# Performance work log

Hardware: AMD Instinct MI355X
Metric: run time of the kernel (lower is better)

The kernel has to match this reference:

```python
import jax, jax.numpy as jnp
import numpy as np

N_NODES = 50000
N_EDGES = 800000
F_IN = 256
HID = 128
HEADS = 4
F_OUT = 64
NEG_SLOPE = 0.2


def setup_inputs() -> dict:
    key = jax.random.key(0)
    ks = jax.random.split(key, 12)
    x = jax.random.normal(ks[0], (N_NODES, F_IN), dtype=jnp.float32)
    edge_index = jax.random.randint(ks[1], (2, N_EDGES), 0, N_NODES, dtype=jnp.int64)
    s = 0.05
    return {
        "x": x,
        "edge_index": edge_index,
        "W1": jax.random.normal(ks[2], (F_IN, HEADS * HID), dtype=jnp.float32) * s,
        "a_src1": jax.random.normal(ks[3], (HEADS, HID), dtype=jnp.float32) * s,
        "a_dst1": jax.random.normal(ks[4], (HEADS, HID), dtype=jnp.float32) * s,
        "b1": jnp.zeros((HEADS * HID,), dtype=jnp.float32),
        "W2": jax.random.normal(ks[5], (HEADS * HID, F_OUT), dtype=jnp.float32) * s,
        "a_src2": jax.random.normal(ks[6], (1, F_OUT), dtype=jnp.float32) * s,
        "a_dst2": jax.random.normal(ks[7], (1, F_OUT), dtype=jnp.float32) * s,
        "b2": jnp.zeros((F_OUT,), dtype=jnp.float32),
    }


def _add_self_loops(edge_index, n):
    loop = jnp.arange(n, dtype=edge_index.dtype)
    return jnp.concatenate([edge_index, jnp.stack([loop, loop])], axis=1)


def _gat_conv(x, edge_index, W, a_src, a_dst, bias, heads, out_ch):
    # PyG GATConv: h = x @ W reshaped to [N, H, C]
    n = x.shape[0]
    h = (x @ W).reshape(n, heads, out_ch)
    # per-node attention logits [N, H]
    al_src = jnp.einsum('nhc,hc->nh', h, a_src)
    al_dst = jnp.einsum('nhc,hc->nh', h, a_dst)
    src, dst = edge_index[0], edge_index[1]
    e = jax.nn.leaky_relu(al_src[src] + al_dst[dst], NEG_SLOPE)  # [E, H]
    # softmax over incoming edges per destination node (segment softmax)
    e_max = jax.ops.segment_max(e, dst, num_segments=n)
    e_exp = jnp.exp(e - e_max[dst])
    denom = jax.ops.segment_sum(e_exp, dst, num_segments=n)
    alpha = e_exp / (denom[dst] + 1e-16)  # [E, H]
    msg = h[src] * alpha[:, :, None]  # [E, H, C]
    out = jax.ops.segment_sum(msg, dst, num_segments=n)  # [N, H, C]
    return out.reshape(n, heads * out_ch) + bias


def reference(x, edge_index, W1, a_src1, a_dst1, b1, W2, a_src2, a_dst2, b2):
    # Dropout layers are identity in eval mode.
    ei = _add_self_loops(edge_index, x.shape[0])
    h = jax.nn.elu(_gat_conv(x, ei, W1, a_src1, a_dst1, b1, HEADS, HID))
    out = _gat_conv(h, ei, W2, a_src2, a_dst2, b2, 1, F_OUT)
    return out
```

## Files before the change

kernel.cpp:

```cpp
#include <hip/hip_runtime.h>
#include <math.h>

#define N_NODES 50000
#define N_EDGES 800000
#define E_TOT   850000
#define F_IN    256
#define F1      512
#define HID     128
#define HEADS   4
#define F_OUT   64

typedef __attribute__((ext_vector_type(8))) short short8;
typedef __attribute__((ext_vector_type(4))) float f32x4;
typedef unsigned short ushort_t;
typedef unsigned int uint_t;

__device__ __forceinline__ float lrelu(float x){ return x > 0.f ? x : 0.2f*x; }
__device__ __forceinline__ float elu(float x){ return x > 0.f ? x : expm1f(x); }

__device__ __forceinline__ ushort_t f2b(float f){
  uint_t u = __builtin_bit_cast(uint_t, f);
  u += 0x7fffu + ((u >> 16) & 1u);
  return (ushort_t)(u >> 16);
}
__device__ __forceinline__ float blo(uint_t u){ return __builtin_bit_cast(float, u << 16); }
__device__ __forceinline__ float bhi(uint_t u){ return __builtin_bit_cast(float, u & 0xffff0000u); }
__device__ __forceinline__ float b2f(ushort_t s){ return __builtin_bit_cast(float, (uint_t)s << 16); }

__global__ void hist_kernel(const int* __restrict__ ei, int* __restrict__ deg16){
  int e = blockIdx.x*blockDim.x + threadIdx.x;
  if (e >= E_TOT) return;
  int dst = (e < N_EDGES) ? ei[N_EDGES + e] : (e - N_EDGES);
  atomicAdd(&deg16[dst*16], 1);
}

__global__ __launch_bounds__(256) void scan1_kernel(const int* __restrict__ deg16,
                                                    int* __restrict__ offs,
                                                    int* __restrict__ bsum){
  __shared__ int sd[256];
  const int tid = threadIdx.x;
  const int i = blockIdx.x*256 + tid;
  int v = (i < N_NODES) ? deg16[i*16] : 0;
  sd[tid] = v; __syncthreads();
  #pragma unroll
  for (int off = 1; off < 256; off <<= 1){
    int t = (tid >= off) ? sd[tid - off] : 0;
    __syncthreads();
    sd[tid] += t;
    __syncthreads();
  }
  if (i < N_NODES) offs[i] = sd[tid] - v;
  if (tid == 255) bsum[blockIdx.x] = sd[255];
}

__global__ __launch_bounds__(256) void scan2_kernel(const int* __restrict__ bsum,
                                                    int* __restrict__ bbase, int nb){
  __shared__ int sd[256];
  const int tid = threadIdx.x;
  int v = (tid < nb) ? bsum[tid] : 0;
  sd[tid] = v; __syncthreads();
  #pragma unroll
  for (int off = 1; off < 256; off <<= 1){
    int t = (tid >= off) ? sd[tid - off] : 0;
    __syncthreads();
    sd[tid] += t;
    __syncthreads();
  }
  if (tid < nb) bbase[tid] = sd[tid] - v;
}

__global__ __launch_bounds__(256) void scan3_kernel(int* __restrict__ offs,
                                                    const int* __restrict__ bbase,
                                                    int* __restrict__ cur16){
  const int i = blockIdx.x*256 + threadIdx.x;
  if (i < N_NODES){
    int o = offs[i] + bbase[blockIdx.x];
    offs[i] = o;
    cur16[i*16] = o;
  }
  if (blockIdx.x == 0 && threadIdx.x == 0) offs[N_NODES] = E_TOT;
}

__global__ void scatter_kernel(const int* __restrict__ ei, int* __restrict__ cur16,
                               int* __restrict__ ssrc){
  int e = blockIdx.x*blockDim.x + threadIdx.x;
  if (e >= E_TOT) return;
  int src, dst;
  if (e < N_EDGES){ src = ei[e]; dst = ei[N_EDGES + e]; }
  else            { src = e - N_EDGES; dst = src; }
  int pos = atomicAdd(&cur16[dst*16], 1);
  ssrc[pos] = src;
}

__global__ __launch_bounds__(256) void cvt_x_kernel(const float* __restrict__ x,
                                                    ushort_t* __restrict__ xb){
  const int t = blockIdx.x*256 + threadIdx.x;
  const float4 a = ((const float4*)x)[t*2];
  const float4 b = ((const float4*)x)[t*2 + 1];
  uint4 o;
  o.x = (uint_t)f2b(a.x) | ((uint_t)f2b(a.y) << 16);
  o.y = (uint_t)f2b(a.z) | ((uint_t)f2b(a.w) << 16);
  o.z = (uint_t)f2b(b.x) | ((uint_t)f2b(b.y) << 16);
  o.w = (uint_t)f2b(b.z) | ((uint_t)f2b(b.w) << 16);
  ((uint4*)xb)[t] = o;
}

__global__ __launch_bounds__(256) void transpose_bf16_kernel(const float* __restrict__ W,
                                                             ushort_t* __restrict__ Wt,
                                                             int K, int N){
  __shared__ float tile[64][65];
  const int k0 = blockIdx.x*64, n0 = blockIdx.y*64;
  const int c = threadIdx.x & 63, r4 = threadIdx.x >> 6;
  for (int r = r4; r < 64; r += 4)
    tile[r][c] = W[(size_t)(k0 + r)*N + n0 + c];
  __syncthreads();
  for (int r = r4; r < 64; r += 4)
    Wt[(size_t)(n0 + r)*K + k0 + c] = f2b(tile[c][r]);
}

template<int K, int WR, int WC>
__global__ __launch_bounds__(256) void gemm_bf16(const ushort_t* __restrict__ A,
                                                 const ushort_t* __restrict__ Bt,
                                                 ushort_t* __restrict__ C,
                                                 int M, int N){
  constexpr int BM = WR*64, BN = WC*64, BKP = 40;
  __shared__ ushort_t As[BM*BKP];
  __shared__ ushort_t Bs[BN*BKP];
  const int tid = threadIdx.x;
  const int wave = tid >> 6, lane = tid & 63, quad = lane >> 4, l16 = lane & 15;
  const int wm = wave % WR, wn = wave / WR;
  const int m0 = blockIdx.x*BM, n0 = blockIdx.y*BN;
  f32x4 acc[4][4] = {};
  for (int k0 = 0; k0 < K; k0 += 32){
    #pragma unroll
    for (int s = tid; s < BM*4; s += 256){
      int r = s >> 2, c = s & 3;
      int gr = m0 + r; if (gr >= M) gr = M - 1;
      *(uint4*)(As + r*BKP + c*8) = *(const uint4*)(A + (size_t)gr*K + k0 + c*8);
    }
    #pragma unroll
    for (int s = tid; s < BN*4; s += 256){
      int r = s >> 2, c = s & 3;
      *(uint4*)(Bs + r*BKP + c*8) = *(const uint4*)(Bt + (size_t)(n0 + r)*K + k0 + c*8);
    }
    __syncthreads();
    short8 af[4], bfr[4];
    #pragma unroll
    for (int i = 0; i < 4; ++i)
      af[i] = *(const short8*)(As + (wm*64 + i*16 + l16)*BKP + quad*8);
    #pragma unroll
    for (int j = 0; j < 4; ++j)
      bfr[j] = *(const short8*)(Bs + (wn*64 + j*16 + l16)*BKP + quad*8);
    #pragma unroll
    for (int i = 0; i < 4; ++i)
      #pragma unroll
      for (int j = 0; j < 4; ++j)
        acc[i][j] = __builtin_amdgcn_mfma_f32_16x16x32_bf16(af[i], bfr[j], acc[i][j], 0, 0, 0);
    __syncthreads();
  }
  #pragma unroll
  for (int i = 0; i < 4; ++i){
    #pragma unroll
    for (int r = 0; r < 4; ++r){
      int row = m0 + wm*64 + i*16 + quad*4 + r;
      if (row < M){
        #pragma unroll
        for (int j = 0; j < 4; ++j){
          int col = n0 + wn*64 + j*16 + l16;
          C[(size_t)row*N + col] = f2b(acc[i][j][r]);
        }
      }
    }
  }
}

__global__ __launch_bounds__(128) void logits1_kernel(const ushort_t* __restrict__ h1b,
                                                      const float* __restrict__ a_src,
                                                      const float* __restrict__ a_dst,
                                                      float* __restrict__ als,
                                                      float* __restrict__ ald){
  const int n = blockIdx.x;
  const int tid = threadIdx.x;
  const int head = tid >> 5, p = tid & 31;
  const uint2 v = *(const uint2*)(h1b + (size_t)n*F1 + tid*4);
  float h0 = blo(v.x), h1 = bhi(v.x), h2 = blo(v.y), h3 = bhi(v.y);
  const float4 as = *(const float4*)(a_src + head*HID + p*4);
  const float4 ad = *(const float4*)(a_dst + head*HID + p*4);
  float ds = h0*as.x + h1*as.y + h2*as.z + h3*as.w;
  float dd = h0*ad.x + h1*ad.y + h2*ad.z + h3*ad.w;
  #pragma unroll
  for (int off = 16; off >= 1; off >>= 1){
    ds += __shfl_down(ds, off, 32);
    dd += __shfl_down(dd, off, 32);
  }
  if (p == 0){ als[n*4 + head] = ds; ald[n*4 + head] = dd; }
}

#define FMA8(hv, al) do{ \
  acc[0] = fmaf(blo((hv).x), (al), acc[0]); \
  acc[1] = fmaf(bhi((hv).x), (al), acc[1]); \
  acc[2] = fmaf(blo((hv).y), (al), acc[2]); \
  acc[3] = fmaf(bhi((hv).y), (al), acc[3]); \
  acc[4] = fmaf(blo((hv).z), (al), acc[4]); \
  acc[5] = fmaf(bhi((hv).z), (al), acc[5]); \
  acc[6] = fmaf(blo((hv).w), (al), acc[6]); \
  acc[7] = fmaf(bhi((hv).w), (al), acc[7]); }while(0)

__global__ __launch_bounds__(256) void agg1_kernel(const ushort_t* __restrict__ h1b,
                                                   const float* __restrict__ als,
                                                   const float* __restrict__ ald1,
                                                   const float* __restrict__ b1,
                                                   const int* __restrict__ offs,
                                                   const int* __restrict__ ssrc,
                                                   ushort_t* __restrict__ hb){
  __shared__ int   shsrc[4][64];
  __shared__ float shal[4][64][4];
  const int wave = threadIdx.x >> 6, lane = threadIdx.x & 63;
  const int n = blockIdx.x*4 + wave;
  const int head = lane >> 4;
  const float4 ald = ((const float4*)ald1)[n];
  const int s0 = offs[n], s1 = offs[n+1];
  const int nE = s1 - s0;

  float acc[8] = {0.f,0.f,0.f,0.f,0.f,0.f,0.f,0.f};

  if (nE <= 64){
    float4 a4 = {0.f,0.f,0.f,0.f};
    int sc = 0;
    if (lane < nE){
      sc = ssrc[s0 + lane];
      const float4 as = ((const float4*)als)[sc];
      a4.x = __expf(lrelu(as.x + ald.x));
      a4.y = __expf(lrelu(as.y + ald.y));
      a4.z = __expf(lrelu(as.z + ald.z));
      a4.w = __expf(lrelu(as.w + ald.w));
    }
    shsrc[wave][lane] = sc;
    *(float4*)&shal[wave][lane][0] = a4;

    const ushort_t* hbase = h1b + lane*8;
    const int nE4 = (nE + 3) & ~3;
    float dsum = 0.f;

    uint4 h0  = *(const uint4*)(hbase + ((size_t)shsrc[wave][0] << 9));
    uint4 h1v = *(const uint4*)(hbase + ((size_t)shsrc[wave][1] << 9));
    uint4 h2v = *(const uint4*)(hbase + ((size_t)shsrc[wave][2] << 9));
    uint4 h3v = *(const uint4*)(hbase + ((size_t)shsrc[wave][3] << 9));
    float al0 = shal[wave][0][head];
    float al1 = shal[wave][1][head];
    float al2 = shal[wave][2][head];
    float al3 = shal[wave][3][head];
    for (int k = 0; k < nE4; k += 4){
      uint4 p0 = h0, p1 = h1v, p2 = h2v, p3 = h3v;
      float q0 = 0.f, q1 = 0.f, q2 = 0.f, q3 = 0.f;
      if (k + 4 < nE4){
        p0 = *(const uint4*)(hbase + ((size_t)shsrc[wave][k+4] << 9));
        p1 = *(const uint4*)(hbase + ((size_t)shsrc[wave][k+5] << 9));
        p2 = *(const uint4*)(hbase + ((size_t)shsrc[wave][k+6] << 9));
        p3 = *(const uint4*)(hbase + ((size_t)shsrc[wave][k+7] << 9));
        q0 = shal[wave][k+4][head];
        q1 = shal[wave][k+5][head];
        q2 = shal[wave][k+6][head];
        q3 = shal[wave][k+7][head];
      }
      dsum += (al0 + al1) + (al2 + al3);
      FMA8(h0,  al0);
      FMA8(h1v, al1);
      FMA8(h2v, al2);
      FMA8(h3v, al3);
      h0 = p0; h1v = p1; h2v = p2; h3v = p3;
      al0 = q0; al1 = q1; al2 = q2; al3 = q3;
    }

    const float rd = 1.0f / (dsum + 1e-16f);
    const float4 ba = *(const float4*)(b1 + lane*8);
    const float4 bb = *(const float4*)(b1 + lane*8 + 4);
    float o0 = elu(fmaf(acc[0], rd, ba.x)), o1 = elu(fmaf(acc[1], rd, ba.y));
    float o2 = elu(fmaf(acc[2], rd, ba.z)), o3 = elu(fmaf(acc[3], rd, ba.w));
    float o4 = elu(fmaf(acc[4], rd, bb.x)), o5 = elu(fmaf(acc[5], rd, bb.y));
    float o6 = elu(fmaf(acc[6], rd, bb.z)), o7 = elu(fmaf(acc[7], rd, bb.w));
    uint4 o;
    o.x = (uint_t)f2b(o0) | ((uint_t)f2b(o1) << 16);
    o.y = (uint_t)f2b(o2) | ((uint_t)f2b(o3) << 16);
    o.z = (uint_t)f2b(o4) | ((uint_t)f2b(o5) << 16);
    o.w = (uint_t)f2b(o6) | ((uint_t)f2b(o7) << 16);
    *(uint4*)(hb + (size_t)n*F1 + lane*8) = o;
    return;
  }

  float d0 = 0.f, d1 = 0.f, d2 = 0.f, d3 = 0.f;
  for (int e = s0 + lane; e < s1; e += 64){
    const int sc = ssrc[e];
    const float4 as = ((const float4*)als)[sc];
    d0 += __expf(lrelu(as.x + ald.x));
    d1 += __expf(lrelu(as.y + ald.y));
    d2 += __expf(lrelu(as.z + ald.z));
    d3 += __expf(lrelu(as.w + ald.w));
  }
  #pragma unroll
  for (int off = 32; off >= 1; off >>= 1){
    d0 += __shfl_xor(d0, off);
    d1 += __shfl_xor(d1, off);
    d2 += __shfl_xor(d2, off);
    d3 += __shfl_xor(d3, off);
  }
  const float den = (head == 0) ? d0 : (head == 1) ? d1 : (head == 2) ? d2 : d3;
  const float rd = 1.0f / (den + 1e-16f);

  for (int ce = s0; ce < s1; ce += 64){
    const int idx = ce + lane;
    if (idx < s1){
      const int sc = ssrc[idx];
      const float4 as = ((const float4*)als)[sc];
      shsrc[wave][lane] = sc;
      float4 a4;
      a4.x = __expf(lrelu(as.x + ald.x));
      a4.y = __expf(lrelu(as.y + ald.y));
      a4.z = __expf(lrelu(as.z + ald.z));
      a4.w = __expf(lrelu(as.w + ald.w));
      *(float4*)&shal[wave][lane][0] = a4;
    }
    const int nB = min(64, s1 - ce);
    for (int k = 0; k < nB; ++k){
      const int scb = shsrc[wave][k];
      const float al = shal[wave][k][head] * rd;
      const uint4 hv = *(const uint4*)(h1b + (size_t)scb*F1 + lane*8);
      FMA8(hv, al);
    }
  }
  const float4 ba = *(const float4*)(b1 + lane*8);
  const float4 bb = *(const float4*)(b1 + lane*8 + 4);
  float o0 = elu(acc[0] + ba.x), o1 = elu(acc[1] + ba.y);
  float o2 = elu(acc[2] + ba.z), o3 = elu(acc[3] + ba.w);
  float o4 = elu(acc[4] + bb.x), o5 = elu(acc[5] + bb.y);
  float o6 = elu(acc[6] + bb.z), o7 = elu(acc[7] + bb.w);
  uint4 o;
  o.x = (uint_t)f2b(o0) | ((uint_t)f2b(o1) << 16);
  o.y = (uint_t)f2b(o2) | ((uint_t)f2b(o3) << 16);
  o.z = (uint_t)f2b(o4) | ((uint_t)f2b(o5) << 16);
  o.w = (uint_t)f2b(o6) | ((uint_t)f2b(o7) << 16);
  *(uint4*)(hb + (size_t)n*F1 + lane*8) = o;
}

__global__ __launch_bounds__(64) void logits2_kernel(const ushort_t* __restrict__ gb,
                                                     const float* __restrict__ a_src,
                                                     const float* __restrict__ a_dst,
                                                     float* __restrict__ als,
                                                     float* __restrict__ ald){
  const int n = blockIdx.x;
  const int tid = threadIdx.x;
  const float v = b2f(gb[(size_t)n*F_OUT + tid]);
  float ds = v * a_src[tid];
  float dd = v * a_dst[tid];
  #pragma unroll
  for (int off = 32; off >= 1; off >>= 1){
    ds += __shfl_xor(ds, off);
    dd += __shfl_xor(dd, off);
  }
  if (tid == 0){ als[n] = ds; ald[n] = dd; }
}

__global__ __launch_bounds__(256) void agg2_kernel(const ushort_t* __restrict__ gb,
                                                   const float* __restrict__ als,
                                                   const float* __restrict__ ald2,
                                                   const float* __restrict__ b2,
                                                   const int* __restrict__ offs,
                                                   const int* __restrict__ ssrc,
                                                   float* __restrict__ out){
  __shared__ int   shsrc[4][64];
  __shared__ float shal[4][64];
  const int wave = threadIdx.x >> 6, lane = threadIdx.x & 63;
  const int n = blockIdx.x*4 + wave;
  const float ald = ald2[n];
  const int s0 = offs[n], s1 = offs[n+1];
  const int nE = s1 - s0;

  if (nE <= 64){
    float av = 0.f; int sc = 0;
    if (lane < nE){
      sc = ssrc[s0 + lane];
      av = __expf(lrelu(als[sc] + ald));
    }
    shsrc[wave][lane] = sc;
    shal[wave][lane] = av;

    const int half = lane >> 5;
    const int ch2  = lane & 31;
    float acc0 = 0.f, acc1 = 0.f, dsum = 0.f;
    for (int k = half; k < nE; k += 2){
      const int scb  = shsrc[wave][k];
      const float al = shal[wave][k];
      const uint_t v = *(const uint_t*)(gb + ((size_t)scb << 6) + ch2*2);
      acc0 = fmaf(blo(v), al, acc0);
      acc1 = fmaf(bhi(v), al, acc1);
      dsum += al;
    }
    acc0 += __shfl_xor(acc0, 32);
    acc1 += __shfl_xor(acc1, 32);
    dsum += __shfl_xor(dsum, 32);
    const float rd = 1.0f / (dsum + 1e-16f);
    if (lane < 32){
      const float2 bb = *(const float2*)(b2 + ch2*2);
      float2 o2;
      o2.x = fmaf(acc0, rd, bb.x);
      o2.y = fmaf(acc1, rd, bb.y);
      *(float2*)(out + (size_t)n*F_OUT + ch2*2) = o2;
    }
    return;
  }

  float dsum = 0.f;
  for (int e = s0 + lane; e < s1; e += 64)
    dsum += __expf(lrelu(als[ssrc[e]] + ald));
  #pragma unroll
  for (int off = 32; off >= 1; off >>= 1)
    dsum += __shfl_xor(dsum, off);
  const float rd = 1.0f / (dsum + 1e-16f);

  float acc = 0.f;
  for (int ce = s0; ce < s1; ce += 64){
    const int idx = ce + lane;
    if (idx < s1){
      const int sc = ssrc[idx];
      shsrc[wave][lane] = sc;
      shal[wave][lane] = __expf(lrelu(als[sc] + ald)) * rd;
    }
    const int nB = min(64, s1 - ce);
    for (int k = 0; k < nB; ++k){
      const int scb = shsrc[wave][k];
      const float al = shal[wave][k];
      acc = fmaf(b2f(gb[(size_t)scb*F_OUT + lane]), al, acc);
    }
  }
  out[(size_t)n*F_OUT + lane] = acc + b2[lane];
}

#undef FMA8

extern "C" void kernel_launch(void* const* d_in, const int* in_sizes, int n_in,
                              void* d_out, int out_size, void* d_ws, size_t ws_size,
                              hipStream_t stream){
  const float* x      = (const float*)d_in[0];
  const int*   ei     = (const int*)  d_in[1];
  const float* W1     = (const float*)d_in[2];
  const float* a_src1 = (const float*)d_in[3];
  const float* a_dst1 = (const float*)d_in[4];
  const float* b1     = (const float*)d_in[5];
  const float* W2     = (const float*)d_in[6];
  const float* a_src2 = (const float*)d_in[7];
  const float* a_dst2 = (const float*)d_in[8];
  const float* b2     = (const float*)d_in[9];
  float* out = (float*)d_out;

  char* ws = (char*)d_ws;
  ushort_t* h1b  = (ushort_t*)(ws + 0UL);
  ushort_t* hb   = (ushort_t*)(ws + 51200000UL);
  ushort_t* xb   = (ushort_t*)(ws + 102400000UL);
  ushort_t* gb   = (ushort_t*)(ws + 128000000UL);
  ushort_t* W1t  = (ushort_t*)(ws + 134400000UL);
  ushort_t* W2t  = (ushort_t*)(ws + 134662144UL);
  float*    als1 = (float*)   (ws + 134727680UL);
  float*    ald1 = (float*)   (ws + 135527680UL);
  float*    als2 = (float*)   (ws + 136327680UL);
  float*    ald2 = (float*)   (ws + 136527680UL);
  int*      offs = (int*)     (ws + 136927680UL);
  int*      bsum = (int*)     (ws + 137127744UL);
  int*      bbase= (int*)     (ws + 137128544UL);
  int*      ssrc = (int*)     (ws + 137329600UL);

  int*      deg16 = (int*)    (ws + 51200000UL);
  int*      cur16 = (int*)    (ws + 54400000UL);

  hipMemsetAsync(deg16, 0, 3200000, stream);

  const int eb = (E_TOT + 255) / 256;
  const int nb = (N_NODES + 255) / 256;
  hist_kernel   <<<eb, 256, 0, stream>>>(ei, deg16);
  scan1_kernel  <<<nb, 256, 0, stream>>>(deg16, offs, bsum);
  scan2_kernel  <<<1, 256, 0, stream>>>(bsum, bbase, nb);
  scan3_kernel  <<<nb, 256, 0, stream>>>(offs, bbase, cur16);
  scatter_kernel<<<eb, 256, 0, stream>>>(ei, cur16, ssrc);

  cvt_x_kernel        <<<6250, 256, 0, stream>>>(x, xb);
  transpose_bf16_kernel<<<dim3(4, 8), 256, 0, stream>>>(W1, W1t, F_IN, F1);
  transpose_bf16_kernel<<<dim3(8, 1), 256, 0, stream>>>(W2, W2t, F1, F_OUT);

  gemm_bf16<F_IN, 2, 2><<<dim3(391, 4), 256, 0, stream>>>(xb, W1t, h1b, N_NODES, F1);
  logits1_kernel<<<N_NODES, 128, 0, stream>>>(h1b, a_src1, a_dst1, als1, ald1);
  agg1_kernel   <<<12500, 256, 0, stream>>>(h1b, als1, ald1, b1, offs, ssrc, hb);

  gemm_bf16<F1, 4, 1><<<dim3(196, 1), 256, 0, stream>>>(hb, W2t, gb, N_NODES, F_OUT);
  logits2_kernel<<<N_NODES, 64, 0, stream>>>(gb, a_src2, a_dst2, als2, ald2);
  agg2_kernel   <<<12500, 256, 0, stream>>>(gb, als2, ald2, b2, offs, ssrc, out);
}
```

Measured before the change: 475.2 us.

## Split layer-1 aggregation into alpha precompute and channel-sliced gather kernel

Replaces the fused layer-1 attention-aggregation kernel with two kernels. The first computes normalized softmax weights per edge and head into a workspace buffer that reuses the x-bf16 region. The second gathers neighbour features in 64-channel slices, with each block covering 16 nodes for one slice, so each gathered row segment is smaller and there are more independent blocks. The cost is an extra pass that writes and then rereads the alpha array. Each lane also now loads 4 bytes per gathered row instead of 16, which adds load instructions.

```diff
diff --git a/kernel.cpp b/kernel.cpp
--- a/kernel.cpp
+++ b/kernel.cpp
@@ -196,95 +196,43 @@
   if (p == 0){ als[n*4 + head] = ds; ald[n*4 + head] = dd; }
 }
 
-#define FMA8(hv, al) do{ \
-  acc[0] = fmaf(blo((hv).x), (al), acc[0]); \
-  acc[1] = fmaf(bhi((hv).x), (al), acc[1]); \
-  acc[2] = fmaf(blo((hv).y), (al), acc[2]); \
-  acc[3] = fmaf(bhi((hv).y), (al), acc[3]); \
-  acc[4] = fmaf(blo((hv).z), (al), acc[4]); \
-  acc[5] = fmaf(bhi((hv).z), (al), acc[5]); \
-  acc[6] = fmaf(blo((hv).w), (al), acc[6]); \
-  acc[7] = fmaf(bhi((hv).w), (al), acc[7]); }while(0)
-
-__global__ __launch_bounds__(256) void agg1_kernel(const ushort_t* __restrict__ h1b,
-                                                   const float* __restrict__ als,
-                                                   const float* __restrict__ ald1,
-                                                   const float* __restrict__ b1,
-                                                   const int* __restrict__ offs,
-                                                   const int* __restrict__ ssrc,
-                                                   ushort_t* __restrict__ hb){
-  __shared__ int   shsrc[4][64];
-  __shared__ float shal[4][64][4];
+__global__ __launch_bounds__(256) void alpha1_kernel(const float* __restrict__ als,
+                                                     const float* __restrict__ ald1,
+                                                     const int* __restrict__ offs,
+                                                     const int* __restrict__ ssrc,
+                                                     float* __restrict__ alpha){
   const int wave = threadIdx.x >> 6, lane = threadIdx.x & 63;
   const int n = blockIdx.x*4 + wave;
-  const int head = lane >> 4;
   const float4 ald = ((const float4*)ald1)[n];
   const int s0 = offs[n], s1 = offs[n+1];
   const int nE = s1 - s0;
 
-  float acc[8] = {0.f,0.f,0.f,0.f,0.f,0.f,0.f,0.f};
-
   if (nE <= 64){
-    float4 a4 = {0.f,0.f,0.f,0.f};
-    int sc = 0;
-    if (lane < nE){
-      sc = ssrc[s0 + lane];
+    float e0 = 0.f, e1 = 0.f, e2 = 0.f, e3 = 0.f;
+    const int idx = s0 + lane;
+    const bool act = lane < nE;
+    if (act){
+      const int sc = ssrc[idx];
       const float4 as = ((const float4*)als)[sc];
-      a4.x = __expf(lrelu(as.x + ald.x));
-      a4.y = __expf(lrelu(as.y + ald.y));
-      a4.z = __expf(lrelu(as.z + ald.z));
-      a4.w = __expf(lrelu(as.w + ald.w));
-    }
-    shsrc[wave][lane] = sc;
-    *(float4*)&shal[wave][lane][0] = a4;
-
-    const ushort_t* hbase = h1b + lane*8;
-    const int nE4 = (nE + 3) & ~3;
-    float dsum = 0.f;
-
-    uint4 h0  = *(const uint4*)(hbase + ((size_t)shsrc[wave][0] << 9));
-    uint4 h1v = *(const uint4*)(hbase + ((size_t)shsrc[wave][1] << 9));
-    uint4 h2v = *(const uint4*)(hbase + ((size_t)shsrc[wave][2] << 9));
-    uint4 h3v = *(const uint4*)(hbase + ((size_t)shsrc[wave][3] << 9));
-    float al0 = shal[wave][0][head];
-    float al1 = shal[wave][1][head];
-    float al2 = shal[wave][2][head];
-    float al3 = shal[wave][3][head];
-    for (int k = 0; k < nE4; k += 4){
-      uint4 p0 = h0, p1 = h1v, p2 = h2v, p3 = h3v;
-      float q0 = 0.f, q1 = 0.f, q2 = 0.f, q3 = 0.f;
-      if (k + 4 < nE4){
-        p0 = *(const uint4*)(hbase + ((size_t)shsrc[wave][k+4] << 9));
-        p1 = *(const uint4*)(hbase + ((size_t)shsrc[wave][k+5] << 9));
-        p2 = *(const uint4*)(hbase + ((size_t)shsrc[wave][k+6] << 9));
-        p3 = *(const uint4*)(hbase + ((size_t)shsrc[wave][k+7] << 9));
-        q0 = shal[wave][k+4][head];
-        q1 = shal[wave][k+5][head];
-        q2 = shal[wave][k+6][head];
-        q3 = shal[wave][k+7][head];
-      }
-      dsum += (al0 + al1) + (al2 + al3);
-      FMA8(h0,  al0);
-      FMA8(h1v, al1);
-      FMA8(h2v, al2);
-      FMA8(h3v, al3);
-      h0 = p0; h1v = p1; h2v = p2; h3v = p3;
-      al0 = q0; al1 = q1; al2 = q2; al3 = q3;
-    }
-
-    const float rd = 1.0f / (dsum + 1e-16f);
-    const float4 ba = *(const float4*)(b1 + lane*8);
-    const float4 bb = *(const float4*)(b1 + lane*8 + 4);
-    float o0 = elu(fmaf(acc[0], rd, ba.x)), o1 = elu(fmaf(acc[1], rd, ba.y));
-    float o2 = elu(fmaf(acc[2], rd, ba.z)), o3 = elu(fmaf(acc[3], rd, ba.w));
-    float o4 = elu(fmaf(acc[4], rd, bb.x)), o5 = elu(fmaf(acc[5], rd, bb.y));
-    float o6 = elu(fmaf(acc[6], rd, bb.z)), o7 = elu(fmaf(acc[7], rd, bb.w));
-    uint4 o;
-    o.x = (uint_t)f2b(o0) | ((uint_t)f2b(o1) << 16);
-    o.y = (uint_t)f2b(o2) | ((uint_t)f2b(o3) << 16);
-    o.z = (uint_t)f2b(o4) | ((uint_t)f2b(o5) << 16);
-    o.w = (uint_t)f2b(o6) | ((uint_t)f2b(o7) << 16);
-    *(uint4*)(hb + (size_t)n*F1 + lane*8) = o;
+      e0 = __expf(lrelu(as.x + ald.x));
+      e1 = __expf(lrelu(as.y + ald.y));
+      e2 = __expf(lrelu(as.z + ald.z));
+      e3 = __expf(lrelu(as.w + ald.w));
+    }
+    float d0 = e0, d1 = e1, d2 = e2, d3 = e3;
+    #pragma unroll
+    for (int off = 32; off >= 1; off >>= 1){
+      d0 += __shfl_xor(d0, off);
+      d1 += __shfl_xor(d1, off);
+      d2 += __shfl_xor(d2, off);
+      d3 += __shfl_xor(d3, off);
+    }
+    if (act){
+      alpha[0*E_TOT + idx] = e0 / (d0 + 1e-16f);
+      alpha[1*E_TOT + idx] = e1 / (d1 + 1e-16f);
+      alpha[2*E_TOT + idx] = e2 / (d2 + 1e-16f);
+      alpha[3*E_TOT + idx] = e3 / (d3 + 1e-16f);
+    }
     return;
   }
 
@@ -304,42 +252,82 @@
     d2 += __shfl_xor(d2, off);
     d3 += __shfl_xor(d3, off);
   }
-  const float den = (head == 0) ? d0 : (head == 1) ? d1 : (head == 2) ? d2 : d3;
-  const float rd = 1.0f / (den + 1e-16f);
-
-  for (int ce = s0; ce < s1; ce += 64){
-    const int idx = ce + lane;
-    if (idx < s1){
-      const int sc = ssrc[idx];
-      const float4 as = ((const float4*)als)[sc];
-      shsrc[wave][lane] = sc;
-      float4 a4;
-      a4.x = __expf(lrelu(as.x + ald.x));
-      a4.y = __expf(lrelu(as.y + ald.y));
-      a4.z = __expf(lrelu(as.z + ald.z));
-      a4.w = __expf(lrelu(as.w + ald.w));
-      *(float4*)&shal[wave][lane][0] = a4;
-    }
-    const int nB = min(64, s1 - ce);
-    for (int k = 0; k < nB; ++k){
-      const int scb = shsrc[wave][k];
-      const float al = shal[wave][k][head] * rd;
-      const uint4 hv = *(const uint4*)(h1b + (size_t)scb*F1 + lane*8);
-      FMA8(hv, al);
-    }
-  }
-  const float4 ba = *(const float4*)(b1 + lane*8);
-  const float4 bb = *(const float4*)(b1 + lane*8 + 4);
-  float o0 = elu(acc[0] + ba.x), o1 = elu(acc[1] + ba.y);
-  float o2 = elu(acc[2] + ba.z), o3 = elu(acc[3] + ba.w);
-  float o4 = elu(acc[4] + bb.x), o5 = elu(acc[5] + bb.y);
-  float o6 = elu(acc[6] + bb.z), o7 = elu(acc[7] + bb.w);
-  uint4 o;
-  o.x = (uint_t)f2b(o0) | ((uint_t)f2b(o1) << 16);
-  o.y = (uint_t)f2b(o2) | ((uint_t)f2b(o3) << 16);
-  o.z = (uint_t)f2b(o4) | ((uint_t)f2b(o5) << 16);
-  o.w = (uint_t)f2b(o6) | ((uint_t)f2b(o7) << 16);
-  *(uint4*)(hb + (size_t)n*F1 + lane*8) = o;
+  const float r0 = 1.f/(d0+1e-16f), r1 = 1.f/(d1+1e-16f);
+  const float r2 = 1.f/(d2+1e-16f), r3 = 1.f/(d3+1e-16f);
+  for (int e = s0 + lane; e < s1; e += 64){
+    const int sc = ssrc[e];
+    const float4 as = ((const float4*)als)[sc];
+    alpha[0*E_TOT + e] = __expf(lrelu(as.x + ald.x)) * r0;
+    alpha[1*E_TOT + e] = __expf(lrelu(as.y + ald.y)) * r1;
+    alpha[2*E_TOT + e] = __expf(lrelu(as.z + ald.z)) * r2;
+    alpha[3*E_TOT + e] = __expf(lrelu(as.w + ald.w)) * r3;
+  }
+}
+
+__global__ __launch_bounds__(256) void agg1s_kernel(const ushort_t* __restrict__ h1b,
+                                                    const float* __restrict__ alpha,
+                                                    const float* __restrict__ b1,
+                                                    const int* __restrict__ offs,
+                                                    const int* __restrict__ ssrc,
+                                                    ushort_t* __restrict__ hb){
+  __shared__ int   shsrc[4][64];
+  __shared__ float shal[4][64];
+  const int wave = threadIdx.x >> 6, lane = threadIdx.x & 63;
+  const int s = blockIdx.x & 7;
+  const int g = blockIdx.x >> 3;
+  const int head = s >> 1;
+  const float* aplane = alpha + (size_t)head*E_TOT;
+  const int half = lane >> 5, ch2 = lane & 31;
+  const ushort_t* hcol = h1b + s*64 + ch2*2;
+  float2 bb = {0.f, 0.f};
+  if (lane < 32) bb = *(const float2*)(b1 + s*64 + ch2*2);
+
+  #pragma unroll
+  for (int q = 0; q < 4; ++q){
+    const int n = g*16 + wave*4 + q;
+    const int s0 = offs[n], s1v = offs[n+1];
+    const int nE = s1v - s0;
+    float acc0 = 0.f, acc1 = 0.f;
+
+    if (nE <= 64){
+      if (lane < nE){
+        shsrc[wave][lane] = ssrc[s0 + lane];
+        shal[wave][lane]  = aplane[s0 + lane];
+      }
+      for (int k = half; k < nE; k += 2){
+        const int scb  = shsrc[wave][k];
+        const float al = shal[wave][k];
+        const uint_t v = *(const uint_t*)(hcol + ((size_t)scb << 9));
+        acc0 = fmaf(blo(v), al, acc0);
+        acc1 = fmaf(bhi(v), al, acc1);
+      }
+    } else {
+      for (int ce = s0; ce < s1v; ce += 64){
+        const int idx = ce + lane;
+        if (idx < s1v){
+          shsrc[wave][lane] = ssrc[idx];
+          shal[wave][lane]  = aplane[idx];
+        }
+        const int nB = min(64, s1v - ce);
+        for (int k = half; k < nB; k += 2){
+          const int scb  = shsrc[wave][k];
+          const float al = shal[wave][k];
+          const uint_t v = *(const uint_t*)(hcol + ((size_t)scb << 9));
+          acc0 = fmaf(blo(v), al, acc0);
+          acc1 = fmaf(bhi(v), al, acc1);
+        }
+      }
+    }
+
+    acc0 += __shfl_xor(acc0, 32);
+    acc1 += __shfl_xor(acc1, 32);
+    if (lane < 32){
+      const float o0 = elu(acc0 + bb.x);
+      const float o1 = elu(acc1 + bb.y);
+      const uint_t o = (uint_t)f2b(o0) | ((uint_t)f2b(o1) << 16);
+      *(uint_t*)(hb + (size_t)n*F1 + s*64 + ch2*2) = o;
+    }
+  }
 }
 
 __global__ __launch_bounds__(64) void logits2_kernel(const ushort_t* __restrict__ gb,
@@ -434,8 +422,6 @@
   }
   out[(size_t)n*F_OUT + lane] = acc + b2[lane];
 }
-
-#undef FMA8
 
 extern "C" void kernel_launch(void* const* d_in, const int* in_sizes, int n_in,
                               void* d_out, int out_size, void* d_ws, size_t ws_size,
@@ -471,6 +457,8 @@
   int*      deg16 = (int*)    (ws + 51200000UL);
   int*      cur16 = (int*)    (ws + 54400000UL);
 
+  float*    alpha = (float*)  (ws + 102400000UL);
+
   hipMemsetAsync(deg16, 0, 3200000, stream);
 
   const int eb = (E_TOT + 255) / 256;
@@ -487,7 +475,8 @@
 
   gemm_bf16<F_IN, 2, 2><<<dim3(391, 4), 256, 0, stream>>>(xb, W1t, h1b, N_NODES, F1);
   logits1_kernel<<<N_NODES, 128, 0, stream>>>(h1b, a_src1, a_dst1, als1, ald1);
-  agg1_kernel   <<<12500, 256, 0, stream>>>(h1b, als1, ald1, b1, offs, ssrc, hb);
+  alpha1_kernel <<<12500, 256, 0, stream>>>(als1, ald1, offs, ssrc, alpha);
+  agg1s_kernel  <<<25000, 256, 0, stream>>>(h1b, alpha, b1, offs, ssrc, hb);
 
   gemm_bf16<F1, 4, 1><<<dim3(196, 1), 256, 0, stream>>>(hb, W2t, gb, N_NODES, F_OUT);
   logits2_kernel<<<N_NODES, 64, 0, stream>>>(gb, a_src2, a_dst2, als2, ald2);
```

Result: slower. 577.7 us (+21.6%).
